# Optimization experiments

Measured on AMD Instinct MI355X. Metric: run time of the kernel, lower is better.

## Reference

```python
import jax, jax.numpy as jnp
import numpy as np

GRID = 128  # interior volume side
THRESH = 0.05
MAX_IT = 500


def setup_inputs() -> dict:
    key = jax.random.key(0)
    # label volume: 0=background, 1=grey matter (solve domain), 2=source, 3=sink
    image = jax.random.randint(key, (GRID, GRID, GRID), 0, 4).astype(jnp.float32)
    return {"image": image, "source_label": 2, "sink_label": 3}


def reference(image, source_label, sink_label):
    # zero-pad by 1 voxel on all sides (as in the torch module)
    img = jnp.pad(image, 1)
    h, w, d = img.shape
    # over-relaxation parameter recomputed from min dim (module overwrites self.wopt)
    wopt = jnp.float32(2.0 / (1.0 + np.pi / min(h, w, d)))

    # boundary conditions: sink -> 1, source -> 0 (zeros already), elsewhere 0
    init = jnp.where(img == sink_label, 1.0, 0.0).astype(jnp.float32)

    # red/black checkerboard restricted to grey-matter (image==1) cells
    i = jnp.arange(h)[:, None, None]
    j = jnp.arange(w)[None, :, None]
    k = jnp.arange(d)[None, None, :]
    parity = (i + j + k) % 2
    gm = (img == 1)
    black = (jnp.logical_and(parity == 0, gm)).reshape(-1).astype(jnp.float32)
    red = (jnp.logical_and(parity == 1, gm)).reshape(-1).astype(jnp.float32)

    v0 = init.reshape(-1)
    # FAITHFUL to the original raveled-offset choice: +-1, +-h, +-h*w
    # (the torch code ravels with strides (w*d, d, 1) but gathers with h/h*w).
    # For cubic padded grids all masked (interior) cells keep these offsets in-bounds,
    # so jnp.roll's wraparound only touches positions the mask discards.
    offs = (1, h, h * w)

    def nbr_sum(v):  # v[i-1]+v[i+1]+v[i-h]+v[i+h]+v[i-h*w]+v[i+h*w]
        s = jnp.zeros_like(v)
        for o in offs:
            s = s + jnp.roll(v, -o) + jnp.roll(v, o)
        return s

    def sweep(v, mask):
        adj = wopt * mask * (nbr_sum(v) - 6.0 * v) / 6.0
        return v + adj, jnp.sum(jnp.abs(adj))

    def body(state):
        v, it, _ = state
        v, dv_b = sweep(v, black)  # black half-sweep (Gauss-Seidel: reads pre-sweep v)
        v, dv_r = sweep(v, red)    # red half-sweep reads black-updated v
        return v, it + 1, dv_b + dv_r

    def cond(state):
        _, it, dv = state
        # original: run once, then continue while delta_v >= thresh and iterations <= 500
        return jnp.logical_or(it == 0, jnp.logical_and(dv >= THRESH, it <= MAX_IT))

    v, iterations, delta_v = jax.lax.while_loop(
        cond, body, (v0, jnp.int32(0), jnp.float32(0.0))
    )

    laplace_sol = v.reshape(h, w, d)[1:-1, 1:-1, 1:-1]
    return laplace_sol, iterations, delta_v
```

## Files before the change

kernel.cpp:

```cpp
#include <hip/hip_runtime.h>
#include <hip/hip_cooperative_groups.h>

namespace cg = cooperative_groups;
typedef unsigned long long u64;

#define G    128
#define GG   (G * G)
#define P    130
#define P2   (P * P)
#define NPAD (P * P * P)
#define NG   (G * G * G)
#define NB   512
#define NT   256
#define TOT  (NB * NT)
#define CH   (NG / NB)
#define SEG  768
#define NLEAD 8
#define NCH   (NB / NLEAD)

__device__ inline float LDV(const float* p) {
    return __hip_atomic_load((float*)p, __ATOMIC_RELAXED, __HIP_MEMORY_SCOPE_AGENT);
}
__device__ inline void STV(float* p, float x) {
    __hip_atomic_store(p, x, __ATOMIC_RELAXED, __HIP_MEMORY_SCOPE_AGENT);
}
__device__ inline u64 LDF(const u64* p) {
    return __hip_atomic_load((u64*)p, __ATOMIC_RELAXED, __HIP_MEMORY_SCOPE_AGENT);
}

__device__ inline float bred(float x, int t, float* s4) {
    for (int o = 32; o; o >>= 1) x += __shfl_down(x, o, 64);
    __syncthreads();
    if ((t & 63) == 0) s4[t >> 6] = x;
    __syncthreads();
    return ((s4[0] + s4[1]) + s4[2]) + s4[3];
}

__device__ inline float gbar2(u64* __restrict__ leaf, u64* __restrict__ lead,
                              int phase, int b, int t, float part) {
    asm volatile("s_waitcnt vmcnt(0)" ::: "memory");
    __syncthreads();
    const int slot = phase & 1;
    if (t == 0) {
        u64 w = ((u64)(unsigned)phase << 32) | (u64)__float_as_uint(part);
        __hip_atomic_store(&leaf[slot * NB + b], w, __ATOMIC_RELAXED,
                           __HIP_MEMORY_SCOPE_AGENT);
    }
    float lsum = 0.0f;
    if (t < 64) {
        if (b < NLEAD) {
            const u64* lp = &leaf[slot * NB + b * NCH + t];
            u64 w;
            for (;;) {
                w = LDF(lp);
                if ((int)(w >> 32) >= phase) break;
                __builtin_amdgcn_s_sleep(1);
            }
            float x = __uint_as_float((unsigned)w);
            for (int o = 32; o; o >>= 1) x = __fadd_rn(x, __shfl_down(x, o, 64));
            if (t == 0) {
                u64 lw = ((u64)(unsigned)phase << 32) | (u64)__float_as_uint(x);
                __hip_atomic_store(&lead[slot * NLEAD + b], lw, __ATOMIC_RELAXED,
                                   __HIP_MEMORY_SCOPE_AGENT);
            }
        }
        const u64* gp = &lead[slot * NLEAD + (t & 7)];
        u64 w;
        for (;;) {
            w = LDF(gp);
            if (__all((int)(w >> 32) >= phase)) break;
            __builtin_amdgcn_s_sleep(1);
        }
        float pay = __uint_as_float((unsigned)w);
        lsum = __shfl(pay, 0, 64);
        lsum = __fadd_rn(lsum, __shfl(pay, 1, 64));
        lsum = __fadd_rn(lsum, __shfl(pay, 2, 64));
        lsum = __fadd_rn(lsum, __shfl(pay, 3, 64));
        lsum = __fadd_rn(lsum, __shfl(pay, 4, 64));
        lsum = __fadd_rn(lsum, __shfl(pay, 5, 64));
        lsum = __fadd_rn(lsum, __shfl(pay, 6, 64));
        lsum = __fadd_rn(lsum, __shfl(pay, 7, 64));
    }
    __syncthreads();
    return lsum;
}

__global__ __launch_bounds__(NT, 4)
void sor_kernel(const float* __restrict__ img, const int* __restrict__ sinkp,
                float* __restrict__ v, int* __restrict__ listB, int* __restrict__ listR,
                u64* __restrict__ leaf, u64* __restrict__ lead,
                float* __restrict__ out)
{
    cg::grid_group grid = cg::this_grid();
    const int t   = (int)threadIdx.x;
    const int b   = (int)blockIdx.x;
    const int tid = b * NT + t;
    const float wopt  = (float)(2.0 / (1.0 + 3.14159265358979323846 / 130.0));
    const float sinkf = (float)(*sinkp);

    __shared__ float slab[CH];
    __shared__ int   sB[NT], sR[NT];
    __shared__ float s4[4];
    __shared__ int   shN[2];

    if (t == 0) {
        __hip_atomic_store(&leaf[b],      0ull, __ATOMIC_RELAXED, __HIP_MEMORY_SCOPE_AGENT);
        __hip_atomic_store(&leaf[NB + b], 0ull, __ATOMIC_RELAXED, __HIP_MEMORY_SCOPE_AGENT);
        if (b < NLEAD) {
            __hip_atomic_store(&lead[b],         0ull, __ATOMIC_RELAXED, __HIP_MEMORY_SCOPE_AGENT);
            __hip_atomic_store(&lead[NLEAD + b], 0ull, __ATOMIC_RELAXED, __HIP_MEMORY_SCOPE_AGENT);
        }
    }

    for (int p = tid; p < NPAD; p += TOT) {
        int i = p / P2;
        int r = p - i * P2;
        int j = r / P;
        int k = r - j * P;
        float vv = 0.0f;
        if (i > 0 && i < P - 1 && j > 0 && j < P - 1 && k > 0 && k < P - 1) {
            float lab = img[(i - 1) * GG + (j - 1) * G + (k - 1)];
            vv = (lab == sinkf) ? 1.0f : 0.0f;
        }
        v[p] = vv;
    }

    for (int x = t; x < CH; x += NT) slab[x] = 0.0f;

    const int g0 = b * CH + t * (CH / NT);
    int cB = 0, cR = 0;
    for (int q = 0; q < CH / NT; ++q) {
        float lab = img[g0 + q];
        if (lab == 1.0f) {
            int g = g0 + q;
            int par = ((g >> 14) + ((g >> 7) & 127) + (g & 127)) & 1;
            if (par) cB++; else cR++;
        }
    }
    sB[t] = cB; sR[t] = cR;
    __syncthreads();
    for (int off = 1; off < NT; off <<= 1) {
        int aB = 0, aR = 0;
        if (t >= off) { aB = sB[t - off]; aR = sR[t - off]; }
        __syncthreads();
        if (t >= off) { sB[t] += aB; sR[t] += aR; }
        __syncthreads();
    }
    const int exB = sB[t] - cB;
    const int exR = sR[t] - cR;
    if (t == NT - 1) { shN[0] = sB[t]; shN[1] = sR[t]; }
    __syncthreads();
    const int cntB = shN[0], cntR = shN[1];

    {
        int pB = exB, pR = exR;
        for (int q = 0; q < CH / NT; ++q) {
            int g = g0 + q;
            float lab = img[g];
            if (lab == 1.0f) {
                int l = t * (CH / NT) + q;
                int i = g >> 14, j = (g >> 7) & 127, k = g & 127;
                if ((i + j + k) & 1) { if (pB < SEG) listB[b * SEG + pB] = l; pB++; }
                else                 { if (pR < SEG) listR[b * SEG + pR] = l; pR++; }
            }
        }
    }
    __syncthreads();

    grid.sync();

#define HOIST(LIST, CNT, X, PV, LV, MV, SV)                                 \
    {                                                                       \
        PV = -1; LV = 0; MV = 0; SV = 0.0f;                                 \
        if ((X) < (CNT)) {                                                  \
            const int l = LIST[b * SEG + (X)]; LV = l;                      \
            const int g = b * CH + l;                                       \
            const int i = g >> 14, j = (g >> 7) & 127, k = g & 127;         \
            PV = (i + 1) * P2 + (j + 1) * P + (k + 1);                      \
            int m = 0; float ss = 0.0f; float lb;                           \
            if (k < 127) { lb = img[g + 1];                                 \
                if (lb == 1.0f) m |= 1;                                     \
                else ss = __fadd_rn(ss, (lb == sinkf) ? 1.0f : 0.0f); }     \
            if (k > 0)   { lb = img[g - 1];                                 \
                if (lb == 1.0f) m |= 2;                                     \
                else ss = __fadd_rn(ss, (lb == sinkf) ? 1.0f : 0.0f); }     \
            if (j < 127) { lb = img[g + G];                                 \
                if (lb == 1.0f) m |= ((j & 31) != 31) ? 4 : 16;             \
                else ss = __fadd_rn(ss, (lb == sinkf) ? 1.0f : 0.0f); }     \
            if (j > 0)   { lb = img[g - G];                                 \
                if (lb == 1.0f) m |= ((j & 31) != 0) ? 8 : 32;              \
                else ss = __fadd_rn(ss, (lb == sinkf) ? 1.0f : 0.0f); }     \
            if (i < 127) { lb = img[g + GG];                                \
                if (lb == 1.0f) m |= 64;                                    \
                else ss = __fadd_rn(ss, (lb == sinkf) ? 1.0f : 0.0f); }     \
            if (i > 0)   { lb = img[g - GG];                                \
                if (lb == 1.0f) m |= 128;                                   \
                else ss = __fadd_rn(ss, (lb == sinkf) ? 1.0f : 0.0f); }     \
            MV = m; SV = ss;                                                \
        }                                                                   \
    }

    int pB0, lB0, mB0; float sB0;
    int pB1, lB1, mB1; float sB1;
    int pB2, lB2, mB2; float sB2;
    int pR0, lR0, mR0; float sR0;
    int pR1, lR1, mR1; float sR1;
    int pR2, lR2, mR2; float sR2;
    HOIST(listB, cntB, t,          pB0, lB0, mB0, sB0)
    HOIST(listB, cntB, t + NT,     pB1, lB1, mB1, sB1)
    HOIST(listB, cntB, t + 2 * NT, pB2, lB2, mB2, sB2)
    HOIST(listR, cntR, t,          pR0, lR0, mR0, sR0)
    HOIST(listR, cntR, t + NT,     pR1, lR1, mR1, sR1)
    HOIST(listR, cntR, t + 2 * NT, pR2, lR2, mR2, sR2)

    float vB0 = 0.0f, vB1 = 0.0f, vB2 = 0.0f;
    float vR0 = 0.0f, vR1 = 0.0f, vR2 = 0.0f;

#define CELLS(PV, LV, MV, SV, V, loc)                                       \
    {                                                                       \
        float xk1 = slab[(LV + 1) & (CH - 1)];                              \
        float xk0 = slab[(LV - 1) & (CH - 1)];                              \
        float xj1 = slab[(LV + G) & (CH - 1)];                              \
        float xj0 = slab[(LV - G) & (CH - 1)];                              \
        float a0 = (MV & 1) ? xk1 : 0.0f;                                   \
        float a1 = (MV & 2) ? xk0 : 0.0f;                                   \
        float a2 = (MV & 4) ? xj1 : ((MV & 16) ? LDV(&v[PV + P]) : 0.0f);   \
        float a3 = (MV & 8) ? xj0 : ((MV & 32) ? LDV(&v[PV - P]) : 0.0f);   \
        float a4 = (MV & 64)  ? LDV(&v[PV + P2]) : 0.0f;                    \
        float a5 = (MV & 128) ? LDV(&v[PV - P2]) : 0.0f;                    \
        float s = __fadd_rn(a0, a1);                                        \
        s = __fadd_rn(s, a2); s = __fadd_rn(s, a3);                         \
        s = __fadd_rn(s, a4); s = __fadd_rn(s, a5);                         \
        s = __fadd_rn(s, SV);                                               \
        float tt = __fsub_rn(s, __fmul_rn(6.0f, V));                        \
        float adj = __fdiv_rn(__fmul_rn(wopt, tt), 6.0f);                   \
        V = __fadd_rn(V, adj);                                              \
        if (PV >= 0) {                                                      \
            slab[LV] = V;                                                   \
            if (MV & 0xF0) STV(&v[PV], V);                                  \
        }                                                                   \
        loc = __fadd_rn(loc, fabsf(adj));                                   \
    }

    int it = 0;
    float dv = 0.0f;
    int phase = 0;
    do {
        float locb = 0.0f;
        CELLS(pB0, lB0, mB0, sB0, vB0, locb)
        CELLS(pB1, lB1, mB1, sB1, vB1, locb)
        CELLS(pB2, lB2, mB2, sB2, vB2, locb)
        float bs = bred(locb, t, s4);
        ++phase;
        float bacc = gbar2(leaf, lead, phase, b, t, bs);

        float locr = 0.0f;
        CELLS(pR0, lR0, mR0, sR0, vR0, locr)
        CELLS(pR1, lR1, mR1, sR1, vR1, locr)
        CELLS(pR2, lR2, mR2, sR2, vR2, locr)
        float rs = bred(locr, t, s4);
        ++phase;
        float racc = gbar2(leaf, lead, phase, b, t, rs);

        if (t == 0) s4[0] = __fadd_rn(bacc, racc);
        __syncthreads();
        dv = s4[0];

        ++it;
    } while (dv >= 0.05f && it <= 500);

    if (pB0 >= 0 && !(mB0 & 0xF0)) STV(&v[pB0], vB0);
    if (pB1 >= 0 && !(mB1 & 0xF0)) STV(&v[pB1], vB1);
    if (pB2 >= 0 && !(mB2 & 0xF0)) STV(&v[pB2], vB2);
    if (pR0 >= 0 && !(mR0 & 0xF0)) STV(&v[pR0], vR0);
    if (pR1 >= 0 && !(mR1 & 0xF0)) STV(&v[pR1], vR1);
    if (pR2 >= 0 && !(mR2 & 0xF0)) STV(&v[pR2], vR2);
    ++phase;
    gbar2(leaf, lead, phase, b, t, 0.0f);

    for (int g = tid; g < NG; g += TOT) {
        int i = g >> 14, j = (g >> 7) & 127, k = g & 127;
        out[g] = LDV(&v[(i + 1) * P2 + (j + 1) * P + (k + 1)]);
    }
    if (tid == 0) {
        out[NG]     = (float)it;
        out[NG + 1] = dv;
    }
}

extern "C" void kernel_launch(void* const* d_in, const int* in_sizes, int n_in,
                              void* d_out, int out_size, void* d_ws, size_t ws_size,
                              hipStream_t stream) {
    const float* img  = (const float*)d_in[0];
    const int*   sink = (const int*)d_in[2];
    float*       out  = (float*)d_out;

    char* ws = (char*)d_ws;
    size_t off = 0;
    float* v = (float*)(ws + off);
    off += (size_t)NPAD * sizeof(float);
    off = (off + 255) & ~(size_t)255;
    int* listB = (int*)(ws + off);
    off += (size_t)NB * SEG * sizeof(int);
    int* listR = (int*)(ws + off);
    off += (size_t)NB * SEG * sizeof(int);
    off = (off + 255) & ~(size_t)255;
    u64* leaf = (u64*)(ws + off);
    off += (size_t)2 * NB * sizeof(u64);
    off = (off + 255) & ~(size_t)255;
    u64* lead = (u64*)(ws + off);
    off += (size_t)2 * NLEAD * sizeof(u64);
    (void)ws_size; (void)in_sizes; (void)n_in; (void)out_size;

    void* args[] = { (void*)&img, (void*)&sink, (void*)&v,
                     (void*)&listB, (void*)&listR,
                     (void*)&leaf, (void*)&lead, (void*)&out };
    hipLaunchCooperativeKernel((const void*)sor_kernel, dim3(NB), dim3(NT),
                               args, 0, stream);
}
```

Baseline: 6.313 ms.

## Replace compacted cell lists with dense per-thread row tiles and bitmask masks

Drops the per-block prefix-scan compaction of grey-matter cells into lists. Each block now owns one i-plane slice of 32 rows, and each thread owns a fixed set of 8 same-parity cells per colour, with neighbour masks packed into a 64-bit word. The slab in shared memory is padded to 129 floats per row, and the final output is written straight from the slab instead of through a global barrier and a reread of v. Off-block neighbour loads are issued in a batch ahead of the compute to overlap latency. The cost is that threads also process inactive cells, and more registers are used per thread.

```diff
diff --git a/kernel.cpp b/kernel.cpp
--- a/kernel.cpp
+++ b/kernel.cpp
@@ -13,10 +13,10 @@
 #define NB   512
 #define NT   256
 #define TOT  (NB * NT)
-#define CH   (NG / NB)
-#define SEG  768
 #define NLEAD 8
 #define NCH   (NB / NLEAD)
+#define SROW 129
+#define SLSZ (34 * SROW)
 
 __device__ inline float LDV(const float* p) {
     return __hip_atomic_load((float*)p, __ATOMIC_RELAXED, __HIP_MEMORY_SCOPE_AGENT);
@@ -87,21 +87,20 @@
 
 __global__ __launch_bounds__(NT, 4)
 void sor_kernel(const float* __restrict__ img, const int* __restrict__ sinkp,
-                float* __restrict__ v, int* __restrict__ listB, int* __restrict__ listR,
-                u64* __restrict__ leaf, u64* __restrict__ lead,
-                float* __restrict__ out)
+                float* __restrict__ v, u64* __restrict__ leaf,
+                u64* __restrict__ lead, float* __restrict__ out)
 {
     cg::grid_group grid = cg::this_grid();
-    const int t   = (int)threadIdx.x;
-    const int b   = (int)blockIdx.x;
-    const int tid = b * NT + t;
+    const int t  = (int)threadIdx.x;
+    const int b  = (int)blockIdx.x;
     const float wopt  = (float)(2.0 / (1.0 + 3.14159265358979323846 / 130.0));
     const float sinkf = (float)(*sinkp);
 
-    __shared__ float slab[CH];
-    __shared__ int   sB[NT], sR[NT];
+    const int i  = b >> 2;
+    const int j0 = (b & 3) << 5;
+
+    __shared__ float slab[SLSZ];
     __shared__ float s4[4];
-    __shared__ int   shN[2];
 
     if (t == 0) {
         __hip_atomic_store(&leaf[b],      0ull, __ATOMIC_RELAXED, __HIP_MEMORY_SCOPE_AGENT);
@@ -112,134 +111,109 @@
         }
     }
 
-    for (int p = tid; p < NPAD; p += TOT) {
-        int i = p / P2;
-        int r = p - i * P2;
-        int j = r / P;
-        int k = r - j * P;
+    for (int p = b * NT + t; p < NPAD; p += TOT) {
+        int pi = p / P2;
+        int rr = p - pi * P2;
+        int pj = rr / P;
+        int pk = rr - pj * P;
         float vv = 0.0f;
-        if (i > 0 && i < P - 1 && j > 0 && j < P - 1 && k > 0 && k < P - 1) {
-            float lab = img[(i - 1) * GG + (j - 1) * G + (k - 1)];
+        if (pi > 0 && pi < P - 1 && pj > 0 && pj < P - 1 && pk > 0 && pk < P - 1) {
+            float lab = img[(pi - 1) * GG + (pj - 1) * G + (pk - 1)];
             vv = (lab == sinkf) ? 1.0f : 0.0f;
         }
         v[p] = vv;
     }
 
-    for (int x = t; x < CH; x += NT) slab[x] = 0.0f;
-
-    const int g0 = b * CH + t * (CH / NT);
-    int cB = 0, cR = 0;
-    for (int q = 0; q < CH / NT; ++q) {
-        float lab = img[g0 + q];
-        if (lab == 1.0f) {
-            int g = g0 + q;
-            int par = ((g >> 14) + ((g >> 7) & 127) + (g & 127)) & 1;
-            if (par) cB++; else cR++;
-        }
-    }
-    sB[t] = cB; sR[t] = cR;
-    __syncthreads();
-    for (int off = 1; off < NT; off <<= 1) {
-        int aB = 0, aR = 0;
-        if (t >= off) { aB = sB[t - off]; aR = sR[t - off]; }
-        __syncthreads();
-        if (t >= off) { sB[t] += aB; sR[t] += aR; }
-        __syncthreads();
-    }
-    const int exB = sB[t] - cB;
-    const int exR = sR[t] - cR;
-    if (t == NT - 1) { shN[0] = sB[t]; shN[1] = sR[t]; }
-    __syncthreads();
-    const int cntB = shN[0], cntR = shN[1];
-
-    {
-        int pB = exB, pR = exR;
-        for (int q = 0; q < CH / NT; ++q) {
-            int g = g0 + q;
-            float lab = img[g];
-            if (lab == 1.0f) {
-                int l = t * (CH / NT) + q;
-                int i = g >> 14, j = (g >> 7) & 127, k = g & 127;
-                if ((i + j + k) & 1) { if (pB < SEG) listB[b * SEG + pB] = l; pB++; }
-                else                 { if (pR < SEG) listR[b * SEG + pR] = l; pR++; }
-            }
-        }
-    }
-    __syncthreads();
+    for (int x = t; x < 32 * G; x += NT) {
+        int r = x >> 7, k = x & 127;
+        float lab = img[i * GG + (j0 + r) * G + k];
+        slab[(r + 1) * SROW + k] = (lab == sinkf) ? 1.0f : 0.0f;
+    }
+
+    const int m  = t & 7;
+    const int r  = t >> 3;
+    const int rp = r + 1;
+    const int j  = j0 + r;
+    const int gb = i * GG + j * G;
+    const int pb = (i + 1) * P2 + (j + 1) * P + 1;
+    const int kbB = (i + j + 1) & 1;
+    const int kbR = (i + j) & 1;
+
+    u64 mB = 0, mR = 0;
+    unsigned actB = 0, actR = 0;
+    float ssB[8], ssR[8];
+
+#define BUILD(KB, MM, ACT, SS)                                              \
+    _Pragma("unroll")                                                       \
+    for (int s = 0; s < 8; ++s) {                                           \
+        const int k = 2 * (m + 8 * s) + (KB);                               \
+        const int g = gb + k;                                               \
+        unsigned mb = 0; float ss = 0.0f; float lb;                         \
+        if (img[g] == 1.0f) ACT |= (1u << s);                               \
+        if (k < 127) { lb = img[g + 1];                                     \
+            if (lb == 1.0f) mb |= 1;                                        \
+            else ss = __fadd_rn(ss, (lb == sinkf) ? 1.0f : 0.0f); }         \
+        if (k > 0)   { lb = img[g - 1];                                     \
+            if (lb == 1.0f) mb |= 2;                                        \
+            else ss = __fadd_rn(ss, (lb == sinkf) ? 1.0f : 0.0f); }         \
+        if (j < 127) { lb = img[g + G];                                     \
+            if (lb == 1.0f) mb |= (r < 31) ? 4u : 16u;                      \
+            else ss = __fadd_rn(ss, (lb == sinkf) ? 1.0f : 0.0f); }         \
+        if (j > 0)   { lb = img[g - G];                                     \
+            if (lb == 1.0f) mb |= (r > 0) ? 8u : 32u;                       \
+            else ss = __fadd_rn(ss, (lb == sinkf) ? 1.0f : 0.0f); }         \
+        if (i < 127) { lb = img[g + GG];                                    \
+            if (lb == 1.0f) mb |= 64;                                       \
+            else ss = __fadd_rn(ss, (lb == sinkf) ? 1.0f : 0.0f); }         \
+        if (i > 0)   { lb = img[g - GG];                                    \
+            if (lb == 1.0f) mb |= 128;                                      \
+            else ss = __fadd_rn(ss, (lb == sinkf) ? 1.0f : 0.0f); }         \
+        MM |= ((u64)mb) << (8 * s);                                         \
+        SS[s] = ss;                                                         \
+    }
+
+    BUILD(kbB, mB, actB, ssB)
+    BUILD(kbR, mR, actR, ssR)
 
     grid.sync();
 
-#define HOIST(LIST, CNT, X, PV, LV, MV, SV)                                 \
+#define SWEEP(KB, MM, ACT, SS, loc)                                         \
     {                                                                       \
-        PV = -1; LV = 0; MV = 0; SV = 0.0f;                                 \
-        if ((X) < (CNT)) {                                                  \
-            const int l = LIST[b * SEG + (X)]; LV = l;                      \
-            const int g = b * CH + l;                                       \
-            const int i = g >> 14, j = (g >> 7) & 127, k = g & 127;         \
-            PV = (i + 1) * P2 + (j + 1) * P + (k + 1);                      \
-            int m = 0; float ss = 0.0f; float lb;                           \
-            if (k < 127) { lb = img[g + 1];                                 \
-                if (lb == 1.0f) m |= 1;                                     \
-                else ss = __fadd_rn(ss, (lb == sinkf) ? 1.0f : 0.0f); }     \
-            if (k > 0)   { lb = img[g - 1];                                 \
-                if (lb == 1.0f) m |= 2;                                     \
-                else ss = __fadd_rn(ss, (lb == sinkf) ? 1.0f : 0.0f); }     \
-            if (j < 127) { lb = img[g + G];                                 \
-                if (lb == 1.0f) m |= ((j & 31) != 31) ? 4 : 16;             \
-                else ss = __fadd_rn(ss, (lb == sinkf) ? 1.0f : 0.0f); }     \
-            if (j > 0)   { lb = img[g - G];                                 \
-                if (lb == 1.0f) m |= ((j & 31) != 0) ? 8 : 32;              \
-                else ss = __fadd_rn(ss, (lb == sinkf) ? 1.0f : 0.0f); }     \
-            if (i < 127) { lb = img[g + GG];                                \
-                if (lb == 1.0f) m |= 64;                                    \
-                else ss = __fadd_rn(ss, (lb == sinkf) ? 1.0f : 0.0f); }     \
-            if (i > 0)   { lb = img[g - GG];                                \
-                if (lb == 1.0f) m |= 128;                                   \
-                else ss = __fadd_rn(ss, (lb == sinkf) ? 1.0f : 0.0f); }     \
-            MV = m; SV = ss;                                                \
+        float la2[8], la3[8], la4[8], la5[8];                               \
+        _Pragma("unroll")                                                   \
+        for (int s = 0; s < 8; ++s) {                                       \
+            const unsigned mb = (unsigned)((MM >> (8 * s)) & 0xff);         \
+            const int p = pb + 2 * (m + 8 * s) + (KB);                      \
+            la2[s] = (mb & 16)  ? LDV(&v[p + P])  : 0.0f;                   \
+            la3[s] = (mb & 32)  ? LDV(&v[p - P])  : 0.0f;                   \
+            la4[s] = (mb & 64)  ? LDV(&v[p + P2]) : 0.0f;                   \
+            la5[s] = (mb & 128) ? LDV(&v[p - P2]) : 0.0f;                   \
         }                                                                   \
-    }
-
-    int pB0, lB0, mB0; float sB0;
-    int pB1, lB1, mB1; float sB1;
-    int pB2, lB2, mB2; float sB2;
-    int pR0, lR0, mR0; float sR0;
-    int pR1, lR1, mR1; float sR1;
-    int pR2, lR2, mR2; float sR2;
-    HOIST(listB, cntB, t,          pB0, lB0, mB0, sB0)
-    HOIST(listB, cntB, t + NT,     pB1, lB1, mB1, sB1)
-    HOIST(listB, cntB, t + 2 * NT, pB2, lB2, mB2, sB2)
-    HOIST(listR, cntR, t,          pR0, lR0, mR0, sR0)
-    HOIST(listR, cntR, t + NT,     pR1, lR1, mR1, sR1)
-    HOIST(listR, cntR, t + 2 * NT, pR2, lR2, mR2, sR2)
-
-    float vB0 = 0.0f, vB1 = 0.0f, vB2 = 0.0f;
-    float vR0 = 0.0f, vR1 = 0.0f, vR2 = 0.0f;
-
-#define CELLS(PV, LV, MV, SV, V, loc)                                       \
-    {                                                                       \
-        float xk1 = slab[(LV + 1) & (CH - 1)];                              \
-        float xk0 = slab[(LV - 1) & (CH - 1)];                              \
-        float xj1 = slab[(LV + G) & (CH - 1)];                              \
-        float xj0 = slab[(LV - G) & (CH - 1)];                              \
-        float a0 = (MV & 1) ? xk1 : 0.0f;                                   \
-        float a1 = (MV & 2) ? xk0 : 0.0f;                                   \
-        float a2 = (MV & 4) ? xj1 : ((MV & 16) ? LDV(&v[PV + P]) : 0.0f);   \
-        float a3 = (MV & 8) ? xj0 : ((MV & 32) ? LDV(&v[PV - P]) : 0.0f);   \
-        float a4 = (MV & 64)  ? LDV(&v[PV + P2]) : 0.0f;                    \
-        float a5 = (MV & 128) ? LDV(&v[PV - P2]) : 0.0f;                    \
-        float s = __fadd_rn(a0, a1);                                        \
-        s = __fadd_rn(s, a2); s = __fadd_rn(s, a3);                         \
-        s = __fadd_rn(s, a4); s = __fadd_rn(s, a5);                         \
-        s = __fadd_rn(s, SV);                                               \
-        float tt = __fsub_rn(s, __fmul_rn(6.0f, V));                        \
-        float adj = __fdiv_rn(__fmul_rn(wopt, tt), 6.0f);                   \
-        V = __fadd_rn(V, adj);                                              \
-        if (PV >= 0) {                                                      \
-            slab[LV] = V;                                                   \
-            if (MV & 0xF0) STV(&v[PV], V);                                  \
+        _Pragma("unroll")                                                   \
+        for (int s = 0; s < 8; ++s) {                                       \
+            const unsigned mb = (unsigned)((MM >> (8 * s)) & 0xff);         \
+            const int k = 2 * (m + 8 * s) + (KB);                           \
+            const int A = rp * SROW + k;                                    \
+            float vc  = slab[A];                                            \
+            float xk1 = slab[A + 1],    xk0 = slab[A - 1];                  \
+            float xj1 = slab[A + SROW], xj0 = slab[A - SROW];               \
+            float a0 = (mb & 1) ? xk1 : 0.0f;                               \
+            float a1 = (mb & 2) ? xk0 : 0.0f;                               \
+            float a2 = (mb & 4) ? xj1 : la2[s];                             \
+            float a3 = (mb & 8) ? xj0 : la3[s];                             \
+            float su = __fadd_rn(a0, a1);                                   \
+            su = __fadd_rn(su, a2); su = __fadd_rn(su, a3);                 \
+            su = __fadd_rn(su, la4[s]); su = __fadd_rn(su, la5[s]);         \
+            su = __fadd_rn(su, SS[s]);                                      \
+            float tt  = __fsub_rn(su, __fmul_rn(6.0f, vc));                 \
+            float adj = __fdiv_rn(__fmul_rn(wopt, tt), 6.0f);               \
+            float nv  = __fadd_rn(vc, adj);                                 \
+            if ((ACT >> s) & 1) {                                           \
+                slab[A] = nv;                                               \
+                if (mb & 0xF0) STV(&v[pb + k], nv);                         \
+                loc = __fadd_rn(loc, fabsf(adj));                           \
+            }                                                               \
         }                                                                   \
-        loc = __fadd_rn(loc, fabsf(adj));                                   \
     }
 
     int it = 0;
@@ -247,17 +221,13 @@
     int phase = 0;
     do {
         float locb = 0.0f;
-        CELLS(pB0, lB0, mB0, sB0, vB0, locb)
-        CELLS(pB1, lB1, mB1, sB1, vB1, locb)
-        CELLS(pB2, lB2, mB2, sB2, vB2, locb)
+        SWEEP(kbB, mB, actB, ssB, locb)
         float bs = bred(locb, t, s4);
         ++phase;
         float bacc = gbar2(leaf, lead, phase, b, t, bs);
 
         float locr = 0.0f;
-        CELLS(pR0, lR0, mR0, sR0, vR0, locr)
-        CELLS(pR1, lR1, mR1, sR1, vR1, locr)
-        CELLS(pR2, lR2, mR2, sR2, vR2, locr)
+        SWEEP(kbR, mR, actR, ssR, locr)
         float rs = bred(locr, t, s4);
         ++phase;
         float racc = gbar2(leaf, lead, phase, b, t, rs);
@@ -269,20 +239,11 @@
         ++it;
     } while (dv >= 0.05f && it <= 500);
 
-    if (pB0 >= 0 && !(mB0 & 0xF0)) STV(&v[pB0], vB0);
-    if (pB1 >= 0 && !(mB1 & 0xF0)) STV(&v[pB1], vB1);
-    if (pB2 >= 0 && !(mB2 & 0xF0)) STV(&v[pB2], vB2);
-    if (pR0 >= 0 && !(mR0 & 0xF0)) STV(&v[pR0], vR0);
-    if (pR1 >= 0 && !(mR1 & 0xF0)) STV(&v[pR1], vR1);
-    if (pR2 >= 0 && !(mR2 & 0xF0)) STV(&v[pR2], vR2);
-    ++phase;
-    gbar2(leaf, lead, phase, b, t, 0.0f);
-
-    for (int g = tid; g < NG; g += TOT) {
-        int i = g >> 14, j = (g >> 7) & 127, k = g & 127;
-        out[g] = LDV(&v[(i + 1) * P2 + (j + 1) * P + (k + 1)]);
-    }
-    if (tid == 0) {
+    for (int x = t; x < 32 * G; x += NT) {
+        int rr = x >> 7, k = x & 127;
+        out[i * GG + (j0 + rr) * G + k] = slab[(rr + 1) * SROW + k];
+    }
+    if (b == 0 && t == 0) {
         out[NG]     = (float)it;
         out[NG + 1] = dv;
     }
@@ -299,11 +260,6 @@
     size_t off = 0;
     float* v = (float*)(ws + off);
     off += (size_t)NPAD * sizeof(float);
-    off = (off + 255) & ~(size_t)255;
-    int* listB = (int*)(ws + off);
-    off += (size_t)NB * SEG * sizeof(int);
-    int* listR = (int*)(ws + off);
-    off += (size_t)NB * SEG * sizeof(int);
     off = (off + 255) & ~(size_t)255;
     u64* leaf = (u64*)(ws + off);
     off += (size_t)2 * NB * sizeof(u64);
@@ -313,7 +269,6 @@
     (void)ws_size; (void)in_sizes; (void)n_in; (void)out_size;
 
     void* args[] = { (void*)&img, (void*)&sink, (void*)&v,
-                     (void*)&listB, (void*)&listR,
                      (void*)&leaf, (void*)&lead, (void*)&out };
     hipLaunchCooperativeKernel((const void*)sor_kernel, dim3(NB), dim3(NT),
                                args, 0, stream);
```

Measured after the change: 15.08 ms. 2.39x slower.

## Drop shared slab, prefetch in-plane neighbors during barrier, write output directly

Applied to the files above, without the earlier changes.

The LDS slab of block-local values goes away. Every grey-matter cell now stores to global v, and the neighbors inside a block's slab are prefetched for the next half-sweep while the split grid barrier is still waiting. Only cross-slab neighbors are loaded after the barrier. The final extra barrier and the gather from the padded v are replaced by each block writing its own output slab from registers. Launch bounds drop to 2 waves per SIMD, and the hoisted setup moves before grid.sync. In exchange there is more global store traffic, and the prefetched values rely on the barrier ordering for correctness.

```diff
diff --git a/kernel.cpp b/kernel.cpp
--- a/kernel.cpp
+++ b/kernel.cpp
@@ -13,7 +13,8 @@
 #define NB   512
 #define NT   256
 #define TOT  (NB * NT)
-#define CH   (NG / NB)
+#define CH   4096
+#define CT   16
 #define SEG  768
 #define NLEAD 8
 #define NCH   (NB / NLEAD)
@@ -36,16 +37,19 @@
     return ((s4[0] + s4[1]) + s4[2]) + s4[3];
 }
 
-__device__ inline float gbar2(u64* __restrict__ leaf, u64* __restrict__ lead,
-                              int phase, int b, int t, float part) {
+__device__ inline void gbar2_begin(u64* __restrict__ leaf, int phase, int b,
+                                   int t, float part) {
     asm volatile("s_waitcnt vmcnt(0)" ::: "memory");
     __syncthreads();
-    const int slot = phase & 1;
     if (t == 0) {
         u64 w = ((u64)(unsigned)phase << 32) | (u64)__float_as_uint(part);
-        __hip_atomic_store(&leaf[slot * NB + b], w, __ATOMIC_RELAXED,
-                           __HIP_MEMORY_SCOPE_AGENT);
-    }
+        __hip_atomic_store(&leaf[(size_t)(phase & 1) * NB + b], w,
+                           __ATOMIC_RELAXED, __HIP_MEMORY_SCOPE_AGENT);
+    }
+}
+__device__ inline float gbar2_end(u64* __restrict__ leaf, u64* __restrict__ lead,
+                                  int phase, int b, int t) {
+    const int slot = phase & 1;
     float lsum = 0.0f;
     if (t < 64) {
         if (b < NLEAD) {
@@ -85,20 +89,22 @@
     return lsum;
 }
 
-__global__ __launch_bounds__(NT, 4)
+__global__ __launch_bounds__(NT, 2)
 void sor_kernel(const float* __restrict__ img, const int* __restrict__ sinkp,
                 float* __restrict__ v, int* __restrict__ listB, int* __restrict__ listR,
                 u64* __restrict__ leaf, u64* __restrict__ lead,
                 float* __restrict__ out)
 {
     cg::grid_group grid = cg::this_grid();
-    const int t   = (int)threadIdx.x;
-    const int b   = (int)blockIdx.x;
-    const int tid = b * NT + t;
+    const int t = (int)threadIdx.x;
+    const int b = (int)blockIdx.x;
     const float wopt  = (float)(2.0 / (1.0 + 3.14159265358979323846 / 130.0));
     const float sinkf = (float)(*sinkp);
 
-    __shared__ float slab[CH];
+    const int i   = b >> 2;
+    const int j0  = (b & 3) << 5;
+    const int gb0 = b * CH;
+
     __shared__ int   sB[NT], sR[NT];
     __shared__ float s4[4];
     __shared__ int   shN[2];
@@ -112,27 +118,23 @@
         }
     }
 
-    for (int p = tid; p < NPAD; p += TOT) {
-        int i = p / P2;
-        int r = p - i * P2;
-        int j = r / P;
-        int k = r - j * P;
+    for (int p = b * NT + t; p < NPAD; p += TOT) {
+        int pi = p / P2;
+        int rr = p - pi * P2;
+        int pj = rr / P;
+        int pk = rr - pj * P;
         float vv = 0.0f;
-        if (i > 0 && i < P - 1 && j > 0 && j < P - 1 && k > 0 && k < P - 1) {
-            float lab = img[(i - 1) * GG + (j - 1) * G + (k - 1)];
+        if (pi > 0 && pi < P - 1 && pj > 0 && pj < P - 1 && pk > 0 && pk < P - 1) {
+            float lab = img[(pi - 1) * GG + (pj - 1) * G + (pk - 1)];
             vv = (lab == sinkf) ? 1.0f : 0.0f;
         }
         v[p] = vv;
     }
 
-    for (int x = t; x < CH; x += NT) slab[x] = 0.0f;
-
-    const int g0 = b * CH + t * (CH / NT);
     int cB = 0, cR = 0;
-    for (int q = 0; q < CH / NT; ++q) {
-        float lab = img[g0 + q];
-        if (lab == 1.0f) {
-            int g = g0 + q;
+    for (int q = 0; q < CT; ++q) {
+        int l = t * CT + q, g = gb0 + l;
+        if (img[g] == 1.0f) {
             int par = ((g >> 14) + ((g >> 7) & 127) + (g & 127)) & 1;
             if (par) cB++; else cR++;
         }
@@ -151,31 +153,26 @@
     if (t == NT - 1) { shN[0] = sB[t]; shN[1] = sR[t]; }
     __syncthreads();
     const int cntB = shN[0], cntR = shN[1];
-
     {
         int pB = exB, pR = exR;
-        for (int q = 0; q < CH / NT; ++q) {
-            int g = g0 + q;
-            float lab = img[g];
-            if (lab == 1.0f) {
-                int l = t * (CH / NT) + q;
-                int i = g >> 14, j = (g >> 7) & 127, k = g & 127;
-                if ((i + j + k) & 1) { if (pB < SEG) listB[b * SEG + pB] = l; pB++; }
-                else                 { if (pR < SEG) listR[b * SEG + pR] = l; pR++; }
+        for (int q = 0; q < CT; ++q) {
+            int l = t * CT + q, g = gb0 + l;
+            if (img[g] == 1.0f) {
+                int par = ((g >> 14) + ((g >> 7) & 127) + (g & 127)) & 1;
+                if (par) { if (pB < SEG) listB[b * SEG + pB] = l; pB++; }
+                else     { if (pR < SEG) listR[b * SEG + pR] = l; pR++; }
             }
         }
     }
     __syncthreads();
 
-    grid.sync();
-
-#define HOIST(LIST, CNT, X, PV, LV, MV, SV)                                 \
+#define HOIST1(LIST, CNT, X, PV, LV, MV, SV)                                \
     {                                                                       \
         PV = -1; LV = 0; MV = 0; SV = 0.0f;                                 \
         if ((X) < (CNT)) {                                                  \
             const int l = LIST[b * SEG + (X)]; LV = l;                      \
-            const int g = b * CH + l;                                       \
-            const int i = g >> 14, j = (g >> 7) & 127, k = g & 127;         \
+            const int j = j0 + (l >> 7), k = l & 127;                       \
+            const int g = gb0 + l;                                          \
             PV = (i + 1) * P2 + (j + 1) * P + (k + 1);                      \
             int m = 0; float ss = 0.0f; float lb;                           \
             if (k < 127) { lb = img[g + 1];                                 \
@@ -185,82 +182,116 @@
                 if (lb == 1.0f) m |= 2;                                     \
                 else ss = __fadd_rn(ss, (lb == sinkf) ? 1.0f : 0.0f); }     \
             if (j < 127) { lb = img[g + G];                                 \
-                if (lb == 1.0f) m |= ((j & 31) != 31) ? 4 : 16;             \
+                if (lb == 1.0f) m |= 4;                                     \
                 else ss = __fadd_rn(ss, (lb == sinkf) ? 1.0f : 0.0f); }     \
             if (j > 0)   { lb = img[g - G];                                 \
-                if (lb == 1.0f) m |= ((j & 31) != 0) ? 8 : 32;              \
+                if (lb == 1.0f) m |= 8;                                     \
                 else ss = __fadd_rn(ss, (lb == sinkf) ? 1.0f : 0.0f); }     \
             if (i < 127) { lb = img[g + GG];                                \
-                if (lb == 1.0f) m |= 64;                                    \
+                if (lb == 1.0f) m |= 16;                                    \
                 else ss = __fadd_rn(ss, (lb == sinkf) ? 1.0f : 0.0f); }     \
             if (i > 0)   { lb = img[g - GG];                                \
-                if (lb == 1.0f) m |= 128;                                   \
-                else ss = __fadd_rn(ss, (lb == sinkf) ? 1.0f : 0.0f); }     \
+                if (lb == 1.0f) m |= 32;                                    \
+                else ss = __fadd_rn(ss, (lb == sinkf) ? 1.0f : 0.0f); }     \
+            if ((l >> 7) == 31) m |= 64;                                    \
+            if ((l >> 7) == 0)  m |= 128;                                   \
             MV = m; SV = ss;                                                \
         }                                                                   \
     }
 
-    int pB0, lB0, mB0; float sB0;
-    int pB1, lB1, mB1; float sB1;
-    int pB2, lB2, mB2; float sB2;
-    int pR0, lR0, mR0; float sR0;
-    int pR1, lR1, mR1; float sR1;
-    int pR2, lR2, mR2; float sR2;
-    HOIST(listB, cntB, t,          pB0, lB0, mB0, sB0)
-    HOIST(listB, cntB, t + NT,     pB1, lB1, mB1, sB1)
-    HOIST(listB, cntB, t + 2 * NT, pB2, lB2, mB2, sB2)
-    HOIST(listR, cntR, t,          pR0, lR0, mR0, sR0)
-    HOIST(listR, cntR, t + NT,     pR1, lR1, mR1, sR1)
-    HOIST(listR, cntR, t + 2 * NT, pR2, lR2, mR2, sR2)
+    int pB0, lB0, mB0; float ssB0;
+    int pB1, lB1, mB1; float ssB1;
+    int pB2, lB2, mB2; float ssB2;
+    int pR0, lR0, mR0; float ssR0;
+    int pR1, lR1, mR1; float ssR1;
+    int pR2, lR2, mR2; float ssR2;
+    HOIST1(listB, cntB, t,          pB0, lB0, mB0, ssB0)
+    HOIST1(listB, cntB, t + NT,     pB1, lB1, mB1, ssB1)
+    HOIST1(listB, cntB, t + 2 * NT, pB2, lB2, mB2, ssB2)
+    HOIST1(listR, cntR, t,          pR0, lR0, mR0, ssR0)
+    HOIST1(listR, cntR, t + NT,     pR1, lR1, mR1, ssR1)
+    HOIST1(listR, cntR, t + 2 * NT, pR2, lR2, mR2, ssR2)
+
+    grid.sync();
+
+#define PRE1(PV, MV, F0, F1, F2, F3)                                        \
+    F0 = (MV & 1) ? LDV(&v[PV + 1]) : 0.0f;                                 \
+    F1 = (MV & 2) ? LDV(&v[PV - 1]) : 0.0f;                                 \
+    F2 = ((MV & (4 | 64))  == 4) ? LDV(&v[PV + P]) : 0.0f;                  \
+    F3 = ((MV & (8 | 128)) == 8) ? LDV(&v[PV - P]) : 0.0f;
+
+#define CROSS1(PV, MV, C2, C3, C4, C5)                                      \
+    C2 = ((MV & (4 | 64))  == (4 | 64))  ? LDV(&v[PV + P])  : 0.0f;         \
+    C3 = ((MV & (8 | 128)) == (8 | 128)) ? LDV(&v[PV - P])  : 0.0f;         \
+    C4 = (MV & 16) ? LDV(&v[PV + P2]) : 0.0f;                               \
+    C5 = (MV & 32) ? LDV(&v[PV - P2]) : 0.0f;
+
+#define CELLX(PV, MV, SV, VV, F0, F1, F2, F3, C2, C3, C4, C5, loc)          \
+    {                                                                       \
+        float a2 = (MV & 64)  ? C2 : F2;                                    \
+        float a3 = (MV & 128) ? C3 : F3;                                    \
+        float su = __fadd_rn(F0, F1);                                       \
+        su = __fadd_rn(su, a2); su = __fadd_rn(su, a3);                     \
+        su = __fadd_rn(su, C4); su = __fadd_rn(su, C5);                     \
+        su = __fadd_rn(su, SV);                                             \
+        float tt  = __fsub_rn(su, __fmul_rn(6.0f, VV));                     \
+        float adj = __fdiv_rn(__fmul_rn(wopt, tt), 6.0f);                   \
+        VV = __fadd_rn(VV, adj);                                            \
+        if (MV & 63) STV(&v[PV], VV);                                       \
+        loc = __fadd_rn(loc, fabsf(adj));                                   \
+    }
 
     float vB0 = 0.0f, vB1 = 0.0f, vB2 = 0.0f;
     float vR0 = 0.0f, vR1 = 0.0f, vR2 = 0.0f;
-
-#define CELLS(PV, LV, MV, SV, V, loc)                                       \
-    {                                                                       \
-        float xk1 = slab[(LV + 1) & (CH - 1)];                              \
-        float xk0 = slab[(LV - 1) & (CH - 1)];                              \
-        float xj1 = slab[(LV + G) & (CH - 1)];                              \
-        float xj0 = slab[(LV - G) & (CH - 1)];                              \
-        float a0 = (MV & 1) ? xk1 : 0.0f;                                   \
-        float a1 = (MV & 2) ? xk0 : 0.0f;                                   \
-        float a2 = (MV & 4) ? xj1 : ((MV & 16) ? LDV(&v[PV + P]) : 0.0f);   \
-        float a3 = (MV & 8) ? xj0 : ((MV & 32) ? LDV(&v[PV - P]) : 0.0f);   \
-        float a4 = (MV & 64)  ? LDV(&v[PV + P2]) : 0.0f;                    \
-        float a5 = (MV & 128) ? LDV(&v[PV - P2]) : 0.0f;                    \
-        float s = __fadd_rn(a0, a1);                                        \
-        s = __fadd_rn(s, a2); s = __fadd_rn(s, a3);                         \
-        s = __fadd_rn(s, a4); s = __fadd_rn(s, a5);                         \
-        s = __fadd_rn(s, SV);                                               \
-        float tt = __fsub_rn(s, __fmul_rn(6.0f, V));                        \
-        float adj = __fdiv_rn(__fmul_rn(wopt, tt), 6.0f);                   \
-        V = __fadd_rn(V, adj);                                              \
-        if (PV >= 0) {                                                      \
-            slab[LV] = V;                                                   \
-            if (MV & 0xF0) STV(&v[PV], V);                                  \
-        }                                                                   \
-        loc = __fadd_rn(loc, fabsf(adj));                                   \
-    }
+    float fB00, fB01, fB02, fB03, fB10, fB11, fB12, fB13, fB20, fB21, fB22, fB23;
+    float fR00, fR01, fR02, fR03, fR10, fR11, fR12, fR13, fR20, fR21, fR22, fR23;
+
+    PRE1(pB0, mB0, fB00, fB01, fB02, fB03)
+    PRE1(pB1, mB1, fB10, fB11, fB12, fB13)
+    PRE1(pB2, mB2, fB20, fB21, fB22, fB23)
+    asm volatile("" ::: "memory");
 
     int it = 0;
     float dv = 0.0f;
     int phase = 0;
     do {
         float locb = 0.0f;
-        CELLS(pB0, lB0, mB0, sB0, vB0, locb)
-        CELLS(pB1, lB1, mB1, sB1, vB1, locb)
-        CELLS(pB2, lB2, mB2, sB2, vB2, locb)
+        {
+            float c02, c03, c04, c05, c12, c13, c14, c15, c22, c23, c24, c25;
+            CROSS1(pB0, mB0, c02, c03, c04, c05)
+            CROSS1(pB1, mB1, c12, c13, c14, c15)
+            CROSS1(pB2, mB2, c22, c23, c24, c25)
+            CELLX(pB0, mB0, ssB0, vB0, fB00, fB01, fB02, fB03, c02, c03, c04, c05, locb)
+            CELLX(pB1, mB1, ssB1, vB1, fB10, fB11, fB12, fB13, c12, c13, c14, c15, locb)
+            CELLX(pB2, mB2, ssB2, vB2, fB20, fB21, fB22, fB23, c22, c23, c24, c25, locb)
+        }
         float bs = bred(locb, t, s4);
         ++phase;
-        float bacc = gbar2(leaf, lead, phase, b, t, bs);
+        gbar2_begin(leaf, phase, b, t, bs);
+        PRE1(pR0, mR0, fR00, fR01, fR02, fR03)
+        PRE1(pR1, mR1, fR10, fR11, fR12, fR13)
+        PRE1(pR2, mR2, fR20, fR21, fR22, fR23)
+        asm volatile("" ::: "memory");
+        float bacc = gbar2_end(leaf, lead, phase, b, t);
 
         float locr = 0.0f;
-        CELLS(pR0, lR0, mR0, sR0, vR0, locr)
-        CELLS(pR1, lR1, mR1, sR1, vR1, locr)
-        CELLS(pR2, lR2, mR2, sR2, vR2, locr)
+        {
+            float c02, c03, c04, c05, c12, c13, c14, c15, c22, c23, c24, c25;
+            CROSS1(pR0, mR0, c02, c03, c04, c05)
+            CROSS1(pR1, mR1, c12, c13, c14, c15)
+            CROSS1(pR2, mR2, c22, c23, c24, c25)
+            CELLX(pR0, mR0, ssR0, vR0, fR00, fR01, fR02, fR03, c02, c03, c04, c05, locr)
+            CELLX(pR1, mR1, ssR1, vR1, fR10, fR11, fR12, fR13, c12, c13, c14, c15, locr)
+            CELLX(pR2, mR2, ssR2, vR2, fR20, fR21, fR22, fR23, c22, c23, c24, c25, locr)
+        }
         float rs = bred(locr, t, s4);
         ++phase;
-        float racc = gbar2(leaf, lead, phase, b, t, rs);
+        gbar2_begin(leaf, phase, b, t, rs);
+        PRE1(pB0, mB0, fB00, fB01, fB02, fB03)
+        PRE1(pB1, mB1, fB10, fB11, fB12, fB13)
+        PRE1(pB2, mB2, fB20, fB21, fB22, fB23)
+        asm volatile("" ::: "memory");
+        float racc = gbar2_end(leaf, lead, phase, b, t);
 
         if (t == 0) s4[0] = __fadd_rn(bacc, racc);
         __syncthreads();
@@ -269,20 +300,18 @@
         ++it;
     } while (dv >= 0.05f && it <= 500);
 
-    if (pB0 >= 0 && !(mB0 & 0xF0)) STV(&v[pB0], vB0);
-    if (pB1 >= 0 && !(mB1 & 0xF0)) STV(&v[pB1], vB1);
-    if (pB2 >= 0 && !(mB2 & 0xF0)) STV(&v[pB2], vB2);
-    if (pR0 >= 0 && !(mR0 & 0xF0)) STV(&v[pR0], vR0);
-    if (pR1 >= 0 && !(mR1 & 0xF0)) STV(&v[pR1], vR1);
-    if (pR2 >= 0 && !(mR2 & 0xF0)) STV(&v[pR2], vR2);
-    ++phase;
-    gbar2(leaf, lead, phase, b, t, 0.0f);
-
-    for (int g = tid; g < NG; g += TOT) {
-        int i = g >> 14, j = (g >> 7) & 127, k = g & 127;
-        out[g] = LDV(&v[(i + 1) * P2 + (j + 1) * P + (k + 1)]);
-    }
-    if (tid == 0) {
+    for (int x = t; x < CH; x += NT) {
+        float lab = img[gb0 + x];
+        out[gb0 + x] = (lab == sinkf) ? 1.0f : 0.0f;
+    }
+    __syncthreads();
+    if (pB0 >= 0) out[gb0 + lB0] = vB0;
+    if (pB1 >= 0) out[gb0 + lB1] = vB1;
+    if (pB2 >= 0) out[gb0 + lB2] = vB2;
+    if (pR0 >= 0) out[gb0 + lR0] = vR0;
+    if (pR1 >= 0) out[gb0 + lR1] = vR1;
+    if (pR2 >= 0) out[gb0 + lR2] = vR2;
+    if (b == 0 && t == 0) {
         out[NG]     = (float)it;
         out[NG + 1] = dv;
     }
```

Measured after the change: 6.986 ms. 10.7% more time.
